# Optimization experiments

Hardware: AMD Instinct MI355X
Metric: run time of the kernel (lower is better)

The kernel has to match this reference:

```python
import jax, jax.numpy as jnp
import numpy as np

B, N, H, L, K = 8, 2048, 256, 4, 16
G, M0, M1, C = 512, 256, 128, 128
EPS = 1e-5


def _rn(k, shape, scale):
    return jax.random.normal(k, shape, jnp.float32) * jnp.float32(scale)


def setup_inputs() -> dict:
    key = jax.random.key(0)
    ks = jax.random.split(key, 16)
    z, o = jnp.zeros, jnp.ones
    return {
        "x": jax.random.normal(ks[0], (B, N, 3), jnp.float32),
        "batch": jnp.repeat(jnp.arange(B, dtype=jnp.int32)[:, None], N, axis=1),
        "Wf": _rn(ks[1], (3, H), 0.5), "bf": z(H),
        "Wnn": _rn(ks[2], (H, H), H ** -0.5), "bnn": z(H),
        "g1": o((L, H)), "b1": z((L, H)),
        "We": _rn(ks[3], (L, 2 * H, H), (2 * H) ** -0.5), "be": z((L, H)),
        "g2": o((L, H)), "b2": z((L, H)),
        "Wl": _rn(ks[4], (L, H, H), H ** -0.5), "bl": z((L, H)),
        "alpha": _rn(ks[5], (L,), 0.1),
        "gg": o(H), "bgb": z(H),
        "Wg": _rn(ks[6], (H, G), H ** -0.5), "bg2": z(G),
        "Wm1": _rn(ks[7], (G, M0), G ** -0.5), "bm1": z(M0),
        "Wm2": _rn(ks[8], (M0, M1), M0 ** -0.5), "bm2": z(M1),
        "Wm3": _rn(ks[9], (M1, C), M1 ** -0.5), "bm3": z(C),
    }


def _bn(x, g, b):
    # BatchNorm1d training-mode math over all nodes (axes B,N), per channel
    m = x.mean(axis=(0, 1))
    v = x.var(axis=(0, 1))
    return (x - m) * jax.lax.rsqrt(v + EPS) * g + b


def _dgcnn(x, We, be):
    # dynamic kNN graph in feature space, per cloud; x: [B,N,H]
    sq = jnp.sum(x * x, axis=-1)                                  # [B,N]
    d = sq[:, :, None] + sq[:, None, :] - 2.0 * jnp.einsum('bnd,bmd->bnm', x, x)
    idx = jax.lax.top_k(-d, K)[1]                                 # [B,N,K] (includes self)
    x_j = jax.vmap(lambda xb, ib: xb[ib])(x, idx)                 # [B,N,K,H]
    x_i = x[:, :, None, :]
    e = jnp.concatenate([jnp.broadcast_to(x_i, x_j.shape), x_j - x_i], axis=-1)
    msg = jnp.einsum('bnkf,fh->bnkh', e, We) + be                 # edge MLP
    return jnp.max(msg, axis=2)                                   # max aggregate


def _forward(x, Wf, bf, Wnn, bnn, g1, b1, We, be, g2, b2, Wl, bl, alpha,
             gg, bgb, Wg, bg2, Wm1, bm1, Wm2, bm2, Wm3, bm3):
    h = x @ Wf + bf                                               # ffm_x (Linear, scale=None)
    for i in range(L):
        t = h @ Wnn + bnn if i == 0 else h                        # nn_x only on first layer
        t = jax.nn.relu(_bn(t, g1[i], b1[i]))
        t = _dgcnn(t, We[i], be[i])
        t = jax.nn.relu(_bn(t, g2[i], b2[i]))
        t = t @ Wl[i] + bl[i]
        h = h + alpha[i] * t                                      # ResidualCoefficient
    t = jax.nn.relu(_bn(h, gg, bgb)) @ Wg + bg2
    p = jnp.max(t, axis=1)                                        # global max pool -> [B,G]
    p = jax.nn.relu(p @ Wm1 + bm1)
    p = jax.nn.relu(p @ Wm2 + bm2)
    return p @ Wm3 + bm3                                          # [B, n_components]


def reference(x, batch, Wf, bf, Wnn, bnn, g1, b1, We, be, g2, b2, Wl, bl, alpha,
              gg, bgb, Wg, bg2, Wm1, bm1, Wm2, bm2, Wm3, bm3):
    # batch ids are implied by the dense [B,N] layout; kept for signature fidelity
    del batch
    return _forward(x, Wf, bf, Wnn, bnn, g1, b1, We, be, g2, b2, Wl, bl, alpha,
                    gg, bgb, Wg, bg2, Wm1, bm1, Wm2, bm2, Wm3, bm3)
```

## Files before the change

kernel.cpp:

```cpp
#include <hip/hip_runtime.h>
#include <cfloat>

#define B_  8
#define N_  2048
#define H_  256
#define L_  4
#define K_  16
#define G_  512
#define M0_ 256
#define M1_ 128
#define C_  128
#define BN_ 16384
#define KP_ 768

typedef unsigned short ushort_t;
typedef __attribute__((ext_vector_type(8))) short short8;
typedef __attribute__((ext_vector_type(4))) float f32x4;

#define OFF_H     ((size_t)0)
#define OFF_APACK ((size_t)16777216)
#define OFF_SQ    ((size_t)67108864)
#define OFF_IDX   ((size_t)67174400)
#define OFF_STATS ((size_t)68222976)
#define OFF_SCSH  ((size_t)68227072)
#define OFF_BCAT  ((size_t)68229120)
#define OFF_P0    ((size_t)68231168)
#define OFF_P1    ((size_t)68247552)
#define OFF_P2    ((size_t)68255744)
#define OFF_D     ((size_t)69206016)
#define OFF_T     (OFF_D + (size_t)0)
#define OFF_UV    (OFF_D + (size_t)50331648)
#define OFF_QW    (OFF_D + (size_t)83886080)
#define OFF_PMAX  (OFF_D + (size_t)84672512)
#define WS_NEEDED ((size_t)203423744)

static __device__ __forceinline__ ushort_t f2bf(float f) {
    unsigned u = __float_as_uint(f);
    unsigned r = (u + 0x7fffu + ((u >> 16) & 1u)) >> 16;
    return (ushort_t)r;
}
static __device__ __forceinline__ float bf2f(ushort_t h) {
    return __uint_as_float(((unsigned)h) << 16);
}
static __device__ __forceinline__ void pack3(float v, ushort_t* A, size_t base, int f) {
    ushort_t hi = f2bf(v);
    ushort_t lo = f2bf(v - bf2f(hi));
    A[base + f] = hi; A[base + H_ + f] = lo; A[base + 2 * H_ + f] = hi;
}


__global__ void feat_pack(const float* __restrict__ x, const float* __restrict__ Wf,
                          const float* __restrict__ bfv, float* __restrict__ h,
                          ushort_t* __restrict__ Ap) {
    int pt = blockIdx.x;
    int f  = threadIdx.x;
    float x0 = x[pt * 3 + 0], x1 = x[pt * 3 + 1], x2 = x[pt * 3 + 2];
    float v = x0 * Wf[f] + x1 * Wf[H_ + f] + x2 * Wf[2 * H_ + f] + bfv[f];
    h[(size_t)pt * H_ + f] = v;
    pack3(v, Ap, (size_t)pt * KP_, f);
}

__global__ void pack_wT(const float* __restrict__ W, ushort_t* __restrict__ Qp, int Nd) {
    int n = blockIdx.x, k = threadIdx.x;
    float w = W[(size_t)k * Nd + n];
    ushort_t hi = f2bf(w), lo = f2bf(w - bf2f(hi));
    size_t base = (size_t)n * KP_;
    Qp[base + k] = hi; Qp[base + H_ + k] = hi; Qp[base + 2 * H_ + k] = lo;
}

__global__ void pack_qcat(const float* __restrict__ We_l, const float* __restrict__ be_l,
                          ushort_t* __restrict__ Qp, float* __restrict__ bcat) {
    int n = blockIdx.x, k = threadIdx.x;
    float w;
    if (n < H_) w = We_l[(size_t)k * H_ + n] - We_l[(size_t)H_ * H_ + (size_t)k * H_ + n];
    else        w = We_l[(size_t)H_ * H_ + (size_t)k * H_ + (n - H_)];
    ushort_t hi = f2bf(w), lo = f2bf(w - bf2f(hi));
    size_t base = (size_t)n * KP_;
    Qp[base + k] = hi; Qp[base + H_ + k] = hi; Qp[base + 2 * H_ + k] = lo;
    if (k == 0) bcat[n] = (n < H_) ? be_l[n] : 0.f;
}

__global__ __launch_bounds__(256) void mfma_gemm(
    const ushort_t* __restrict__ P, const ushort_t* __restrict__ Q,
    const float* __restrict__ aux, float* __restrict__ out,
    int Kd, int ldOut, int mode, const float* __restrict__ resid,
    const float* __restrict__ alphap, int aidx, double* __restrict__ stats,
    int nx) {
    __shared__ __align__(16) ushort_t As[128 * 32];
    __shared__ __align__(16) ushort_t Bs[128 * 32];
    __shared__ float cs1[4][64], cs2[4][64];
    int i0, j0;
    if (nx) {
        int blk = blockIdx.x;
        int z = blk & 7;
        int rest = blk >> 3;
        int xb = rest % nx;
        int ys = rest / nx;
        i0 = (z * 16 + ys) * 128;
        j0 = xb * 128;
    } else {
        i0 = blockIdx.y * 128; j0 = blockIdx.x * 128;
    }
    int tid = threadIdx.x;
    int lane = tid & 63, wave = tid >> 6;
    int wm = wave & 1, wn = wave >> 1;
    int m16 = lane & 15, kq = (lane >> 4) * 8;

    f32x4 acc[4][4];
    f32x4 zero = {0.f, 0.f, 0.f, 0.f};
#pragma unroll
    for (int i = 0; i < 4; ++i)
#pragma unroll
        for (int j = 0; j < 4; ++j) acc[i][j] = zero;

    int srow = tid >> 2;
    int skc  = (tid & 3) * 8;

    for (int k0 = 0; k0 < Kd; k0 += 32) {
#pragma unroll
        for (int s = 0; s < 2; ++s) {
            int row = srow + s * 64;
            const ushort_t* gpA = P + (size_t)(i0 + row) * Kd + k0 + skc;
            const ushort_t* gpB = Q + (size_t)(j0 + row) * Kd + k0 + skc;
            __builtin_amdgcn_global_load_lds(
                (const __attribute__((address_space(1))) void*)gpA,
                (__attribute__((address_space(3))) void*)(As + (size_t)(wave * 64 + s * 256) * 8),
                16, 0, 0);
            __builtin_amdgcn_global_load_lds(
                (const __attribute__((address_space(1))) void*)gpB,
                (__attribute__((address_space(3))) void*)(Bs + (size_t)(wave * 64 + s * 256) * 8),
                16, 0, 0);
        }
        __syncthreads();
        short8 af[4], bfr[4];
#pragma unroll
        for (int fi = 0; fi < 4; ++fi)
            af[fi] = *(const short8*)(As + (wm * 64 + fi * 16 + m16) * 32 + kq);
#pragma unroll
        for (int fj = 0; fj < 4; ++fj)
            bfr[fj] = *(const short8*)(Bs + (wn * 64 + fj * 16 + m16) * 32 + kq);
#pragma unroll
        for (int fi = 0; fi < 4; ++fi)
#pragma unroll
            for (int fj = 0; fj < 4; ++fj)
                acc[fi][fj] = __builtin_amdgcn_mfma_f32_16x16x32_bf16(
                    af[fi], bfr[fj], acc[fi][fj], 0, 0, 0);
        __syncthreads();
    }
    float alpha = (mode == 2) ? alphap[aidx] : 0.f;
    int rbase = i0 + wm * 64 + (lane >> 4) * 4;
    int cbase = j0 + wn * 64 + m16;
    float s1[4] = {0.f, 0.f, 0.f, 0.f}, s2[4] = {0.f, 0.f, 0.f, 0.f};
#pragma unroll
    for (int fi = 0; fi < 4; ++fi) {
#pragma unroll
        for (int fj = 0; fj < 4; ++fj) {
            int c = cbase + fj * 16;
            float a = aux[c];
#pragma unroll
            for (int r = 0; r < 4; ++r) {
                int gr = rbase + fi * 16 + r;
                size_t oidx = (size_t)gr * ldOut + c;
                float val;
                if (mode == 2) val = resid[oidx] + alpha * (acc[fi][fj][r] + a);
                else           val = acc[fi][fj][r] + a;
                out[oidx] = val;
                s1[fj] += val; s2[fj] += val * val;
            }
        }
    }
    if (stats) {
#pragma unroll
        for (int fj = 0; fj < 4; ++fj) {
            float a1 = s1[fj], a2 = s2[fj];
            a1 += __shfl_xor(a1, 16); a1 += __shfl_xor(a1, 32);
            a2 += __shfl_xor(a2, 16); a2 += __shfl_xor(a2, 32);
            if ((lane >> 4) == 0) {
                cs1[wave][fj * 16 + m16] = a1;
                cs2[wave][fj * 16 + m16] = a2;
            }
        }
        __syncthreads();
        if (tid < 128) {
            int wnl = tid >> 6, cl = tid & 63;
            float t1 = cs1[2 * wnl][cl] + cs1[2 * wnl + 1][cl];
            float t2 = cs2[2 * wnl][cl] + cs2[2 * wnl + 1][cl];
            int c = j0 + tid;
            atomicAdd(&stats[c], (double)t1);
            atomicAdd(&stats[H_ + c], (double)t2);
        }
    }
}

__global__ __launch_bounds__(256) void gram_sym(const ushort_t* __restrict__ Ap,
                                                const float* __restrict__ sqb,
                                                float* __restrict__ D) {
    __shared__ __align__(16) ushort_t As[128 * 32];
    __shared__ __align__(16) ushort_t Bs[128 * 32];
    __shared__ __align__(16) float stg[4][1280];
    int blk = blockIdx.x;
    int z = blk & 7;
    int p = blk >> 3;
    int bi = 0, rem = p;
    while (rem >= 16 - bi) { rem -= 16 - bi; ++bi; }
    int bj = bi + rem;
    const ushort_t* Pz = Ap + (size_t)z * N_ * KP_;
    const float* sqz = sqb + (size_t)z * N_;
    float* Dz = D + (size_t)z * N_ * N_;
    int i0 = bi * 128, j0 = bj * 128;

    int tid = threadIdx.x;
    int lane = tid & 63, wave = tid >> 6;
    int wm = wave & 1, wn = wave >> 1;
    int m16 = lane & 15, q4 = lane >> 4;
    int kq = q4 * 8;

    f32x4 acc[4][4];
    f32x4 zero = {0.f, 0.f, 0.f, 0.f};
#pragma unroll
    for (int i = 0; i < 4; ++i)
#pragma unroll
        for (int j = 0; j < 4; ++j) acc[i][j] = zero;

    int srow = tid >> 2;
    int skc  = (tid & 3) * 8;

    for (int k0 = 0; k0 < KP_; k0 += 32) {
        int kb = (k0 < 256) ? k0 : ((k0 < 512) ? k0 + 256 : k0 - 256);
#pragma unroll
        for (int s = 0; s < 2; ++s) {
            int row = srow + s * 64;
            const ushort_t* gpA = Pz + (size_t)(i0 + row) * KP_ + k0 + skc;
            const ushort_t* gpB = Pz + (size_t)(j0 + row) * KP_ + kb + skc;
            __builtin_amdgcn_global_load_lds(
                (const __attribute__((address_space(1))) void*)gpA,
                (__attribute__((address_space(3))) void*)(As + (size_t)(wave * 64 + s * 256) * 8),
                16, 0, 0);
            __builtin_amdgcn_global_load_lds(
                (const __attribute__((address_space(1))) void*)gpB,
                (__attribute__((address_space(3))) void*)(Bs + (size_t)(wave * 64 + s * 256) * 8),
                16, 0, 0);
        }
        __syncthreads();
        short8 af[4], bfr[4];
#pragma unroll
        for (int fi = 0; fi < 4; ++fi)
            af[fi] = *(const short8*)(As + (wm * 64 + fi * 16 + m16) * 32 + kq);
#pragma unroll
        for (int fj = 0; fj < 4; ++fj)
            bfr[fj] = *(const short8*)(Bs + (wn * 64 + fj * 16 + m16) * 32 + kq);
#pragma unroll
        for (int fi = 0; fi < 4; ++fi)
#pragma unroll
            for (int fj = 0; fj < 4; ++fj)
                acc[fi][fj] = __builtin_amdgcn_mfma_f32_16x16x32_bf16(
                    af[fi], bfr[fj], acc[fi][fj], 0, 0, 0);
        __syncthreads();
    }

    float* sg = stg[wave];
    float scl[4];
#pragma unroll
    for (int fj = 0; fj < 4; ++fj) scl[fj] = sqz[j0 + wn * 64 + fj * 16 + m16];
    float sr[4][4];
#pragma unroll
    for (int fi = 0; fi < 4; ++fi) {
        float4 s4 = *(const float4*)(sqz + i0 + wm * 64 + fi * 16 + q4 * 4);
        sr[fi][0] = s4.x; sr[fi][1] = s4.y; sr[fi][2] = s4.z; sr[fi][3] = s4.w;
    }

    int rr = lane >> 2, cc = lane & 3;
#pragma unroll
    for (int fi = 0; fi < 4; ++fi) {
#pragma unroll
        for (int fj = 0; fj < 4; ++fj)
#pragma unroll
            for (int r = 0; r < 4; ++r)
                sg[(q4 * 4 + r) * 68 + fj * 16 + m16] = scl[fj] - 2.f * acc[fi][fj][r];
        float* drow = Dz + (size_t)(i0 + wm * 64 + fi * 16 + rr) * N_ + j0 + wn * 64;
#pragma unroll
        for (int t = 0; t < 4; ++t) {
            int chunk = cc + 4 * t;
            f32x4 o = *(const f32x4*)(sg + rr * 68 + chunk * 4);
            __builtin_nontemporal_store(o, (f32x4*)(drow + chunk * 4));
        }
    }

    if (bi != bj) {
#pragma unroll
        for (int fi = 0; fi < 4; ++fi) {
#pragma unroll
            for (int fj = 0; fj < 4; ++fj)
#pragma unroll
                for (int r = 0; r < 4; ++r)
                    sg[(fj * 16 + m16) * 20 + q4 * 4 + r] =
                        sr[fi][r] - 2.f * acc[fi][fj][r];
            int chunk = lane & 3;
#pragma unroll
            for (int u = 0; u < 4; ++u) {
                int cr = (lane >> 2) + 16 * u;
                f32x4 o = *(const f32x4*)(sg + cr * 20 + chunk * 4);
                __builtin_nontemporal_store(o,
                    (f32x4*)(Dz + (size_t)(j0 + wn * 64 + cr) * N_ +
                             i0 + wm * 64 + fi * 16 + chunk * 4));
            }
        }
    }
}

__global__ __launch_bounds__(256) void topk16(const float* __restrict__ D,
                                              int* __restrict__ idxb) {
    __shared__ unsigned long long cand[4][256];
    __shared__ int cnt[4];
    int w = threadIdx.x >> 6, lane = threadIdx.x & 63;
    int row = blockIdx.x * 4 + w;
    const float* dp = D + (size_t)row * N_;
    unsigned sk[32];
#pragma unroll
    for (int t = 0; t < 8; ++t) {
        f32x4 v4 = __builtin_nontemporal_load((const f32x4*)(dp + t * 256 + lane * 4));
#pragma unroll
        for (int j = 0; j < 4; ++j) {
            unsigned u = __float_as_uint(v4[j]);
            sk[t * 4 + j] = (u & 0x80000000u) ? ~u : (u | 0x80000000u);
        }
    }
    if (lane == 0) cnt[w] = 0;
    unsigned vm = sk[0];
#pragma unroll
    for (int i = 1; i < 32; ++i) vm = min(vm, sk[i]);
#pragma unroll
    for (int k = 2; k <= 64; k <<= 1) {
#pragma unroll
        for (int j = k >> 1; j > 0; j >>= 1) {
            unsigned pv = __shfl_xor(vm, j);
            bool up = ((lane & k) == 0);
            bool lower = ((lane & j) == 0);
            unsigned mn = min(vm, pv), mx = max(vm, pv);
            vm = (lower == up) ? mn : mx;
        }
    }
    unsigned T = __shfl(vm, 15);
    __syncthreads();
#pragma unroll
    for (int i = 0; i < 32; ++i) {
        if (sk[i] <= T) {
            unsigned col = (unsigned)((i >> 2) * 256 + lane * 4 + (i & 3));
            int s = atomicAdd(&cnt[w], 1);
            if (s < 256) cand[w][s] = ((unsigned long long)sk[i] << 32) | col;
        }
    }
    __syncthreads();
    int cn = cnt[w];
    if (cn <= 64) {
        unsigned long long mykey = (lane < cn) ? cand[w][lane] : ~0ull;
        for (int it = 0; it < 16; ++it) {
            unsigned long long best = mykey;
#pragma unroll
            for (int off = 32; off; off >>= 1) {
                unsigned long long o = __shfl_xor(best, off);
                if (o < best) best = o;
            }
            if (mykey == best) mykey = ~0ull;
            if (lane == 0) idxb[row * 16 + it] = (int)(unsigned)(best & 0xffffffffu);
        }
    } else if (cn <= 256) {
        for (int it = 0; it < 16; ++it) {
            unsigned long long best = ~0ull;
            for (int i = lane; i < cn; i += 64) {
                unsigned long long c = cand[w][i];
                if (c < best) best = c;
            }
#pragma unroll
            for (int off = 32; off; off >>= 1) {
                unsigned long long o = __shfl_xor(best, off);
                if (o < best) best = o;
            }
            for (int i = lane; i < cn; i += 64)
                if (cand[w][i] == best) cand[w][i] = ~0ull;
            if (lane == 0) idxb[row * 16 + it] = (int)(unsigned)(best & 0xffffffffu);
        }
    } else {
        unsigned mask = 0;
        for (int it = 0; it < 16; ++it) {
            unsigned long long key = ~0ull;
#pragma unroll
            for (int i = 0; i < 32; ++i) {
                if (!((mask >> i) & 1u)) {
                    unsigned long long k2 = ((unsigned long long)sk[i] << 32) |
                        (unsigned)((i >> 2) * 256 + lane * 4 + (i & 3));
                    if (k2 < key) key = k2;
                }
            }
#pragma unroll
            for (int off = 32; off; off >>= 1) {
                unsigned long long o = __shfl_xor(key, off);
                if (o < key) key = o;
            }
            unsigned jc = (unsigned)(key & 0xffffffffu);
            int li = ((jc & 255) >> 2);
            int ii = ((jc >> 8) << 2) | (jc & 3);
            if (lane == li) mask |= 1u << ii;
            if (lane == 0) idxb[row * 16 + it] = (int)jc;
        }
    }
}

__global__ void gather_max(const float* __restrict__ uv, const int* __restrict__ idxb,
                           float* __restrict__ outp, double* __restrict__ stats) {
    int blk = blockIdx.x;
    int b = blk & 7;
    int strip = blk >> 3;
    int r0 = b * N_ + strip * 32;
    int f = threadIdx.x;
    float s1 = 0.f, s2 = 0.f;
    for (int rr = 0; rr < 32; ++rr) {
        int row = r0 + rr;
        const int* ip = idxb + row * 16;
        float m = -FLT_MAX;
#pragma unroll
        for (int k = 0; k < 16; ++k) {
            int j = ip[k];
            m = fmaxf(m, uv[((size_t)((b << 11) + j)) * 512 + 256 + f]);
        }
        float v = uv[(size_t)row * 512 + f] + m;
        outp[(size_t)row * H_ + f] = v;
        s1 += v; s2 += v * v;
    }
    atomicAdd(&stats[f], (double)s1);
    atomicAdd(&stats[H_ + f], (double)s2);
}

__global__ void bn_zero(double* s) { s[threadIdx.x] = 0.0; }

__global__ void bn_final(double* __restrict__ sums, const float* __restrict__ g,
                         const float* __restrict__ b, float* __restrict__ scsh) {
    int f = threadIdx.x;
    double m  = sums[f] / (double)BN_;
    double var = sums[H_ + f] / (double)BN_ - m * m;
    double inv = 1.0 / sqrt(var + 1e-5);
    float sc = g[f] * (float)inv;
    scsh[f] = sc;
    scsh[H_ + f] = b[f] - (float)m * sc;
    sums[f] = 0.0; sums[H_ + f] = 0.0;
}

__global__ void bn_apply_pack(const float* __restrict__ X, const float* __restrict__ scsh,
                              ushort_t* __restrict__ Ap, float* __restrict__ sq) {
    int tid = threadIdx.x;
    int row = blockIdx.x * 8 + (tid >> 5);
    int f0  = (tid & 31) * 8;
    const float* xp = X + (size_t)row * H_ + f0;
    f32x4 x0 = *(const f32x4*)(xp);
    f32x4 x1 = *(const f32x4*)(xp + 4);
    f32x4 sc0 = *(const f32x4*)(scsh + f0);
    f32x4 sc1 = *(const f32x4*)(scsh + f0 + 4);
    f32x4 sh0 = *(const f32x4*)(scsh + H_ + f0);
    f32x4 sh1 = *(const f32x4*)(scsh + H_ + f0 + 4);
    float v[8];
#pragma unroll
    for (int i = 0; i < 4; ++i) {
        v[i]     = fmaxf(x0[i] * sc0[i] + sh0[i], 0.f);
        v[i + 4] = fmaxf(x1[i] * sc1[i] + sh1[i], 0.f);
    }
    short8 hi8, lo8;
#pragma unroll
    for (int i = 0; i < 8; ++i) {
        ushort_t hi = f2bf(v[i]);
        ushort_t lo = f2bf(v[i] - bf2f(hi));
        hi8[i] = (short)hi; lo8[i] = (short)lo;
    }
    ushort_t* ap = Ap + (size_t)row * KP_ + f0;
    *(short8*)(ap)            = hi8;
    *(short8*)(ap + H_)       = lo8;
    *(short8*)(ap + 2 * H_)   = hi8;
    if (sq) {
        float s = 0.f;
#pragma unroll
        for (int i = 0; i < 8; ++i) s += v[i] * v[i];
#pragma unroll
        for (int off = 16; off; off >>= 1) s += __shfl_down(s, off, 32);
        if ((tid & 31) == 0) sq[row] = s;
    }
}

__global__ void maxpool1(const float* __restrict__ y, float* __restrict__ pmax) {
    int b = blockIdx.x, gc = blockIdx.y, nc = blockIdx.z;
    int g = gc * 256 + threadIdx.x;
    const float* yb = y + ((size_t)b * N_ + (size_t)nc * 128) * G_;
    float m = -FLT_MAX;
    for (int n = 0; n < 128; ++n) m = fmaxf(m, yb[(size_t)n * G_ + g]);
    pmax[((size_t)(b * 16 + nc)) * G_ + g] = m;
}

__global__ void maxpool2(const float* __restrict__ pmax, float* __restrict__ p) {
    int b = blockIdx.x;
    int g = blockIdx.y * 256 + threadIdx.x;
    float m = -FLT_MAX;
    for (int c = 0; c < 16; ++c) m = fmaxf(m, pmax[((size_t)(b * 16 + c)) * G_ + g]);
    p[(size_t)b * G_ + g] = m;
}

__global__ __launch_bounds__(256) void head_gemm(const float* __restrict__ A,
                                                 const float* __restrict__ W,
                                                 const float* __restrict__ bias,
                                                 float* __restrict__ Cc,
                                                 int Kd, int Nd, int relu) {
    int m = blockIdx.x;
    int c0 = blockIdx.y * 64;
    int cl = threadIdx.x & 63;
    int ks = threadIdx.x >> 6;
    int kper = Kd >> 2;
    const float* Ap = A + (size_t)m * Kd + (size_t)ks * kper;
    const float* Wp = W + (size_t)ks * kper * Nd + c0 + cl;
    float acc = 0.f;
    for (int k = 0; k < kper; k += 8) {
#pragma unroll
        for (int u2 = 0; u2 < 8; ++u2)
            acc += Ap[k + u2] * Wp[(size_t)(k + u2) * Nd];
    }
    __shared__ float red[4][64];
    red[ks][cl] = acc;
    __syncthreads();
    if (ks == 0) {
        float s = red[0][cl] + red[1][cl] + red[2][cl] + red[3][cl] + bias[c0 + cl];
        if (relu) s = fmaxf(s, 0.f);
        Cc[(size_t)m * Nd + c0 + cl] = s;
    }
}

extern "C" void kernel_launch(void* const* d_in, const int* in_sizes, int n_in,
                              void* d_out, int out_size, void* d_ws, size_t ws_size,
                              hipStream_t stream) {
    (void)in_sizes; (void)n_in; (void)out_size;
    if (ws_size < WS_NEEDED) return;

    const float* x    = (const float*)d_in[0];
    const float* Wf   = (const float*)d_in[2];
    const float* bfv  = (const float*)d_in[3];
    const float* Wnn  = (const float*)d_in[4];
    const float* bnn  = (const float*)d_in[5];
    const float* g1   = (const float*)d_in[6];
    const float* b1   = (const float*)d_in[7];
    const float* We   = (const float*)d_in[8];
    const float* be   = (const float*)d_in[9];
    const float* g2   = (const float*)d_in[10];
    const float* b2   = (const float*)d_in[11];
    const float* Wl   = (const float*)d_in[12];
    const float* bl   = (const float*)d_in[13];
    const float* alpha= (const float*)d_in[14];
    const float* gg   = (const float*)d_in[15];
    const float* bgb  = (const float*)d_in[16];
    const float* Wg   = (const float*)d_in[17];
    const float* bg2  = (const float*)d_in[18];
    const float* Wm1  = (const float*)d_in[19];
    const float* bm1  = (const float*)d_in[20];
    const float* Wm2  = (const float*)d_in[21];
    const float* bm2  = (const float*)d_in[22];
    const float* Wm3  = (const float*)d_in[23];
    const float* bm3  = (const float*)d_in[24];
    float* outp = (float*)d_out;

    char* ws = (char*)d_ws;
    float*    h    = (float*)(ws + OFF_H);
    ushort_t* Ap   = (ushort_t*)(ws + OFF_APACK);
    float*    sqb  = (float*)(ws + OFF_SQ);
    int*      idxb = (int*)  (ws + OFF_IDX);
    double*   stats= (double*)(ws + OFF_STATS);
    float*    scsh = (float*)(ws + OFF_SCSH);
    float*    bcat = (float*)(ws + OFF_BCAT);
    float*    p0   = (float*)(ws + OFF_P0);
    float*    p1   = (float*)(ws + OFF_P1);
    float*    p2   = (float*)(ws + OFF_P2);
    float*    dmat = (float*)(ws + OFF_D);
    float*    t    = (float*)(ws + OFF_T);
    float*    uv   = (float*)(ws + OFF_UV);
    float*    y    = (float*)(ws + OFF_UV);
    ushort_t* Qw   = (ushort_t*)(ws + OFF_QW);
    float*    pmax = (float*)(ws + OFF_PMAX);

    hipLaunchKernelGGL(bn_zero, dim3(1), dim3(512), 0, stream, stats);

    hipLaunchKernelGGL(feat_pack, dim3(BN_), dim3(256), 0, stream, x, Wf, bfv, h, Ap);
    hipLaunchKernelGGL(pack_wT, dim3(H_), dim3(256), 0, stream, Wnn, Qw, H_);
    hipLaunchKernelGGL(mfma_gemm, dim3(256), dim3(256), 0, stream,
                       Ap, Qw, bnn, t, KP_, H_, 0,
                       (const float*)nullptr, (const float*)nullptr, 0, stats, 2);

    for (int l = 0; l < L_; ++l) {
        const float* src1 = (l == 0) ? t : h;
        hipLaunchKernelGGL(bn_final, dim3(1), dim3(256), 0, stream,
                           stats, g1 + l * H_, b1 + l * H_, scsh);
        hipLaunchKernelGGL(bn_apply_pack, dim3(BN_ / 8), dim3(256), 0, stream,
                           src1, scsh, Ap, sqb);
        hipLaunchKernelGGL(gram_sym, dim3(1088), dim3(256), 0, stream,
                           Ap, sqb, dmat);
        hipLaunchKernelGGL(topk16, dim3(BN_ / 4), dim3(256), 0, stream, dmat, idxb);
        hipLaunchKernelGGL(pack_qcat, dim3(512), dim3(256), 0, stream,
                           We + (size_t)l * 2 * H_ * H_, be + (size_t)l * H_, Qw, bcat);
        hipLaunchKernelGGL(mfma_gemm, dim3(512), dim3(256), 0, stream,
                           Ap, Qw, bcat, uv, KP_, 512, 0,
                           (const float*)nullptr, (const float*)nullptr, 0,
                           (double*)nullptr, 4);
        hipLaunchKernelGGL(gather_max, dim3(512), dim3(256), 0, stream,
                           uv, idxb, t, stats);
        hipLaunchKernelGGL(bn_final, dim3(1), dim3(256), 0, stream,
                           stats, g2 + l * H_, b2 + l * H_, scsh);
        hipLaunchKernelGGL(bn_apply_pack, dim3(BN_ / 8), dim3(256), 0, stream,
                           t, scsh, Ap, (float*)nullptr);
        hipLaunchKernelGGL(pack_wT, dim3(H_), dim3(256), 0, stream,
                           Wl + (size_t)l * H_ * H_, Qw, H_);
        hipLaunchKernelGGL(mfma_gemm, dim3(256), dim3(256), 0, stream,
                           Ap, Qw, bl + (size_t)l * H_, h, KP_, H_, 2,
                           h, alpha, l, stats, 2);
    }

    hipLaunchKernelGGL(bn_final, dim3(1), dim3(256), 0, stream, stats, gg, bgb, scsh);
    hipLaunchKernelGGL(bn_apply_pack, dim3(BN_ / 8), dim3(256), 0, stream,
                       h, scsh, Ap, (float*)nullptr);
    hipLaunchKernelGGL(pack_wT, dim3(G_), dim3(256), 0, stream, Wg, Qw, G_);
    hipLaunchKernelGGL(mfma_gemm, dim3(512), dim3(256), 0, stream,
                       Ap, Qw, bg2, y, KP_, G_, 0,
                       (const float*)nullptr, (const float*)nullptr, 0,
                       (double*)nullptr, 4);
    hipLaunchKernelGGL(maxpool1, dim3(8, 2, 16), dim3(256), 0, stream, y, pmax);
    hipLaunchKernelGGL(maxpool2, dim3(8, 2), dim3(256), 0, stream, pmax, p0);
    hipLaunchKernelGGL(head_gemm, dim3(8, 4), dim3(256), 0, stream, p0, Wm1, bm1, p1, G_, M0_, 1);
    hipLaunchKernelGGL(head_gemm, dim3(8, 2), dim3(256), 0, stream, p1, Wm2, bm2, p2, M0_, M1_, 1);
    hipLaunchKernelGGL(head_gemm, dim3(8, 2), dim3(256), 0, stream, p2, Wm3, bm3, outp, M1_, C_, 0);
}
```

Baseline: 1.135 ms.

## Fuse per-tile top-16 selection into Gram kernel, drop full distance matrix

The Gram kernel no longer writes the full 2048x2048 distance matrix per cloud. Each wave converts its 64x64 tile to sortable keys in shared memory and selects a top-16 candidate set per row with bitonic networks. It then writes compact key and column candidates, which a new topk_cand kernel merges into the final 16 neighbours. This removes the large D write and read traffic in exchange for heavy register use (64-element arrays per lane), a 66 KB dynamic LDS allocation that lowers occupancy, and extra per-tile sorting work.

```diff
diff --git a/kernel.cpp b/kernel.cpp
--- a/kernel.cpp
+++ b/kernel.cpp
@@ -28,6 +28,8 @@
 #define OFF_P1    ((size_t)68247552)
 #define OFF_P2    ((size_t)68255744)
 #define OFF_D     ((size_t)69206016)
+#define OFF_CK    (OFF_D)
+#define OFF_CC    (OFF_D + (size_t)33554432)
 #define OFF_T     (OFF_D + (size_t)0)
 #define OFF_UV    (OFF_D + (size_t)50331648)
 #define OFF_QW    (OFF_D + (size_t)83886080)
@@ -42,10 +44,99 @@
 static __device__ __forceinline__ float bf2f(ushort_t h) {
     return __uint_as_float(((unsigned)h) << 16);
 }
+static __device__ __forceinline__ unsigned f2key(float f) {
+    unsigned u = __float_as_uint(f);
+    return (u & 0x80000000u) ? ~u : (u | 0x80000000u);
+}
 static __device__ __forceinline__ void pack3(float v, ushort_t* A, size_t base, int f) {
     ushort_t hi = f2bf(v);
     ushort_t lo = f2bf(v - bf2f(hi));
     A[base + f] = hi; A[base + H_ + f] = lo; A[base + 2 * H_ + f] = hi;
+}
+
+#define CEA(x, y) { unsigned mn_ = min(x, y), mx_ = max(x, y); (x) = mn_; (y) = mx_; }
+
+static __device__ __forceinline__ void sortnet16(unsigned* s) {
+#pragma unroll
+    for (int k = 2; k <= 16; k <<= 1) {
+#pragma unroll
+        for (int j = k >> 1; j > 0; j >>= 1) {
+#pragma unroll
+            for (int i = 0; i < 16; ++i) {
+                int l = i ^ j;
+                if (l > i) {
+                    if ((i & k) == 0) { CEA(s[i], s[l]); }
+                    else              { CEA(s[l], s[i]); }
+                }
+            }
+        }
+    }
+}
+static __device__ __forceinline__ void clean16(unsigned* s) {
+#pragma unroll
+    for (int j = 8; j > 0; j >>= 1) {
+#pragma unroll
+        for (int i = 0; i < 16; ++i) {
+            int l = i ^ j;
+            if (l > i) { CEA(s[i], s[l]); }
+        }
+    }
+}
+
+static __device__ __forceinline__ void select_emit(
+    unsigned* arena_wave, int lane,
+    unsigned* __restrict__ kc, ushort_t* __restrict__ cc,
+    size_t Rrow, int chunk) {
+    unsigned* mr = arena_wave + lane * 66;
+    unsigned v[64];
+#pragma unroll
+    for (int i = 0; i < 32; ++i) {
+        uint2 t2 = *(const uint2*)(mr + 2 * i);
+        v[2 * i] = t2.x; v[2 * i + 1] = t2.y;
+    }
+    unsigned a[16], b[16], m1[16], m2[16];
+#pragma unroll
+    for (int i = 0; i < 16; ++i) { a[i] = v[i]; b[i] = v[16 + i]; }
+    sortnet16(a); sortnet16(b);
+#pragma unroll
+    for (int i = 0; i < 16; ++i) m1[i] = min(a[i], b[15 - i]);
+    clean16(m1);
+#pragma unroll
+    for (int i = 0; i < 16; ++i) { a[i] = v[32 + i]; b[i] = v[48 + i]; }
+    sortnet16(a); sortnet16(b);
+#pragma unroll
+    for (int i = 0; i < 16; ++i) m2[i] = min(a[i], b[15 - i]);
+    clean16(m2);
+    unsigned T = 0;
+#pragma unroll
+    for (int i = 0; i < 16; ++i) T = max(T, min(m1[i], m2[15 - i]));
+    int cnt = 0;
+#pragma unroll
+    for (int i = 0; i < 64; ++i) {
+        if (v[i] < T) { mr[cnt] = v[i]; mr[16 + cnt] = (unsigned)i; ++cnt; }
+    }
+#pragma unroll
+    for (int i = 0; i < 64; ++i) {
+        if (v[i] == T && cnt < 16) { mr[cnt] = v[i]; mr[16 + cnt] = (unsigned)i; ++cnt; }
+    }
+    unsigned kk[16], c16[16];
+#pragma unroll
+    for (int i = 0; i < 8; ++i) {
+        uint2 tk = *(const uint2*)(mr + 2 * i);
+        kk[2 * i] = tk.x; kk[2 * i + 1] = tk.y;
+        uint2 tc = *(const uint2*)(mr + 16 + 2 * i);
+        c16[2 * i] = tc.x; c16[2 * i + 1] = tc.y;
+    }
+    size_t kb = (Rrow * 32 + (size_t)chunk) * 16;
+    *(uint4*)(kc + kb)      = make_uint4(kk[0],  kk[1],  kk[2],  kk[3]);
+    *(uint4*)(kc + kb + 4)  = make_uint4(kk[4],  kk[5],  kk[6],  kk[7]);
+    *(uint4*)(kc + kb + 8)  = make_uint4(kk[8],  kk[9],  kk[10], kk[11]);
+    *(uint4*)(kc + kb + 12) = make_uint4(kk[12], kk[13], kk[14], kk[15]);
+    unsigned w[8];
+#pragma unroll
+    for (int i = 0; i < 8; ++i) w[i] = c16[2 * i] | (c16[2 * i + 1] << 16);
+    *(uint4*)(cc + kb)     = make_uint4(w[0], w[1], w[2], w[3]);
+    *(uint4*)(cc + kb + 8) = make_uint4(w[4], w[5], w[6], w[7]);
 }
 
 
@@ -194,10 +285,11 @@
 
 __global__ __launch_bounds__(256) void gram_sym(const ushort_t* __restrict__ Ap,
                                                 const float* __restrict__ sqb,
-                                                float* __restrict__ D) {
-    __shared__ __align__(16) ushort_t As[128 * 32];
-    __shared__ __align__(16) ushort_t Bs[128 * 32];
-    __shared__ __align__(16) float stg[4][1280];
+                                                unsigned* __restrict__ kc,
+                                                ushort_t* __restrict__ cc) {
+    extern __shared__ __align__(16) unsigned dyns[];
+    ushort_t* As = (ushort_t*)dyns;
+    ushort_t* Bs = (ushort_t*)dyns + 4096;
     int blk = blockIdx.x;
     int z = blk & 7;
     int p = blk >> 3;
@@ -206,7 +298,6 @@
     int bj = bi + rem;
     const ushort_t* Pz = Ap + (size_t)z * N_ * KP_;
     const float* sqz = sqb + (size_t)z * N_;
-    float* Dz = D + (size_t)z * N_ * N_;
     int i0 = bi * 128, j0 = bj * 128;
 
     int tid = threadIdx.x;
@@ -257,8 +348,8 @@
                     af[fi], bfr[fj], acc[fi][fj], 0, 0, 0);
         __syncthreads();
     }
-
-    float* sg = stg[wave];
+    unsigned* my = dyns + wave * (64 * 66);
+
     float scl[4];
 #pragma unroll
     for (int fj = 0; fj < 4; ++fj) scl[fj] = sqz[j0 + wn * 64 + fj * 16 + m16];
@@ -269,66 +360,56 @@
         sr[fi][0] = s4.x; sr[fi][1] = s4.y; sr[fi][2] = s4.z; sr[fi][3] = s4.w;
     }
 
-    int rr = lane >> 2, cc = lane & 3;
-#pragma unroll
-    for (int fi = 0; fi < 4; ++fi) {
+#pragma unroll
+    for (int fi = 0; fi < 4; ++fi)
 #pragma unroll
         for (int fj = 0; fj < 4; ++fj)
 #pragma unroll
             for (int r = 0; r < 4; ++r)
-                sg[(q4 * 4 + r) * 68 + fj * 16 + m16] = scl[fj] - 2.f * acc[fi][fj][r];
-        float* drow = Dz + (size_t)(i0 + wm * 64 + fi * 16 + rr) * N_ + j0 + wn * 64;
-#pragma unroll
-        for (int t = 0; t < 4; ++t) {
-            int chunk = cc + 4 * t;
-            f32x4 o = *(const f32x4*)(sg + rr * 68 + chunk * 4);
-            __builtin_nontemporal_store(o, (f32x4*)(drow + chunk * 4));
-        }
-    }
+                my[(fi * 16 + q4 * 4 + r) * 66 + (fj * 16 + m16)] =
+                    f2key(scl[fj] - 2.f * acc[fi][fj][r]);
+    select_emit(my, lane, kc, cc,
+                (size_t)z * N_ + i0 + wm * 64 + lane, 2 * bj + wn);
 
     if (bi != bj) {
 #pragma unroll
-        for (int fi = 0; fi < 4; ++fi) {
+        for (int fi = 0; fi < 4; ++fi)
 #pragma unroll
             for (int fj = 0; fj < 4; ++fj)
 #pragma unroll
                 for (int r = 0; r < 4; ++r)
-                    sg[(fj * 16 + m16) * 20 + q4 * 4 + r] =
-                        sr[fi][r] - 2.f * acc[fi][fj][r];
-            int chunk = lane & 3;
-#pragma unroll
-            for (int u = 0; u < 4; ++u) {
-                int cr = (lane >> 2) + 16 * u;
-                f32x4 o = *(const f32x4*)(sg + cr * 20 + chunk * 4);
-                __builtin_nontemporal_store(o,
-                    (f32x4*)(Dz + (size_t)(j0 + wn * 64 + cr) * N_ +
-                             i0 + wm * 64 + fi * 16 + chunk * 4));
-            }
-        }
-    }
-}
-
-__global__ __launch_bounds__(256) void topk16(const float* __restrict__ D,
-                                              int* __restrict__ idxb) {
+                    my[(fj * 16 + m16) * 66 + (fi * 16 + q4 * 4 + r)] =
+                        f2key(sr[fi][r] - 2.f * acc[fi][fj][r]);
+        select_emit(my, lane, kc, cc,
+                    (size_t)z * N_ + j0 + wn * 64 + lane, 2 * bi + wm);
+    }
+}
+
+__global__ __launch_bounds__(256) void topk_cand(const unsigned* __restrict__ kcand,
+                                                 const ushort_t* __restrict__ ccand,
+                                                 int* __restrict__ idxb) {
     __shared__ unsigned long long cand[4][256];
     __shared__ int cnt[4];
     int w = threadIdx.x >> 6, lane = threadIdx.x & 63;
     int row = blockIdx.x * 4 + w;
-    const float* dp = D + (size_t)row * N_;
-    unsigned sk[32];
-#pragma unroll
-    for (int t = 0; t < 8; ++t) {
-        f32x4 v4 = __builtin_nontemporal_load((const f32x4*)(dp + t * 256 + lane * 4));
-#pragma unroll
-        for (int j = 0; j < 4; ++j) {
-            unsigned u = __float_as_uint(v4[j]);
-            sk[t * 4 + j] = (u & 0x80000000u) ? ~u : (u | 0x80000000u);
-        }
+    const unsigned* kp = kcand + (size_t)row * 512 + lane * 8;
+    uint4 ka = *(const uint4*)(kp);
+    uint4 kb = *(const uint4*)(kp + 4);
+    unsigned sk[8] = {ka.x, ka.y, ka.z, ka.w, kb.x, kb.y, kb.z, kb.w};
+    const ushort_t* cp = ccand + (size_t)row * 512 + lane * 8;
+    uint4 cw = *(const uint4*)(cp);
+    unsigned cwa[4] = {cw.x, cw.y, cw.z, cw.w};
+    unsigned colbase = (unsigned)(lane >> 1) * 64u;
+    unsigned long long k2[8];
+#pragma unroll
+    for (int j = 0; j < 8; ++j) {
+        unsigned c = colbase + ((cwa[j >> 1] >> ((j & 1) * 16)) & 0xffffu);
+        k2[j] = ((unsigned long long)sk[j] << 32) | c;
     }
     if (lane == 0) cnt[w] = 0;
     unsigned vm = sk[0];
 #pragma unroll
-    for (int i = 1; i < 32; ++i) vm = min(vm, sk[i]);
+    for (int i = 1; i < 8; ++i) vm = min(vm, sk[i]);
 #pragma unroll
     for (int k = 2; k <= 64; k <<= 1) {
 #pragma unroll
@@ -343,11 +424,10 @@
     unsigned T = __shfl(vm, 15);
     __syncthreads();
 #pragma unroll
-    for (int i = 0; i < 32; ++i) {
-        if (sk[i] <= T) {
-            unsigned col = (unsigned)((i >> 2) * 256 + lane * 4 + (i & 3));
+    for (int j = 0; j < 8; ++j) {
+        if (sk[j] <= T) {
             int s = atomicAdd(&cnt[w], 1);
-            if (s < 256) cand[w][s] = ((unsigned long long)sk[i] << 32) | col;
+            if (s < 256) cand[w][s] = k2[j];
         }
     }
     __syncthreads();
@@ -381,27 +461,21 @@
             if (lane == 0) idxb[row * 16 + it] = (int)(unsigned)(best & 0xffffffffu);
         }
     } else {
-        unsigned mask = 0;
+        unsigned msk = 0;
         for (int it = 0; it < 16; ++it) {
             unsigned long long key = ~0ull;
 #pragma unroll
-            for (int i = 0; i < 32; ++i) {
-                if (!((mask >> i) & 1u)) {
-                    unsigned long long k2 = ((unsigned long long)sk[i] << 32) |
-                        (unsigned)((i >> 2) * 256 + lane * 4 + (i & 3));
-                    if (k2 < key) key = k2;
-                }
-            }
+            for (int i = 0; i < 8; ++i)
+                if (!((msk >> i) & 1u) && k2[i] < key) key = k2[i];
 #pragma unroll
             for (int off = 32; off; off >>= 1) {
                 unsigned long long o = __shfl_xor(key, off);
                 if (o < key) key = o;
             }
-            unsigned jc = (unsigned)(key & 0xffffffffu);
-            int li = ((jc & 255) >> 2);
-            int ii = ((jc >> 8) << 2) | (jc & 3);
-            if (lane == li) mask |= 1u << ii;
-            if (lane == 0) idxb[row * 16 + it] = (int)jc;
+#pragma unroll
+            for (int i = 0; i < 8; ++i)
+                if (k2[i] == key) msk |= 1u << i;
+            if (lane == 0) idxb[row * 16 + it] = (int)(unsigned)(key & 0xffffffffu);
         }
     }
 }
@@ -572,7 +646,8 @@
     float*    p0   = (float*)(ws + OFF_P0);
     float*    p1   = (float*)(ws + OFF_P1);
     float*    p2   = (float*)(ws + OFF_P2);
-    float*    dmat = (float*)(ws + OFF_D);
+    unsigned* kcand= (unsigned*)(ws + OFF_CK);
+    ushort_t* ccand= (ushort_t*)(ws + OFF_CC);
     float*    t    = (float*)(ws + OFF_T);
     float*    uv   = (float*)(ws + OFF_UV);
     float*    y    = (float*)(ws + OFF_UV);
@@ -593,9 +668,10 @@
                            stats, g1 + l * H_, b1 + l * H_, scsh);
         hipLaunchKernelGGL(bn_apply_pack, dim3(BN_ / 8), dim3(256), 0, stream,
                            src1, scsh, Ap, sqb);
-        hipLaunchKernelGGL(gram_sym, dim3(1088), dim3(256), 0, stream,
-                           Ap, sqb, dmat);
-        hipLaunchKernelGGL(topk16, dim3(BN_ / 4), dim3(256), 0, stream, dmat, idxb);
+        hipLaunchKernelGGL(gram_sym, dim3(1088), dim3(256), 67584, stream,
+                           Ap, sqb, kcand, ccand);
+        hipLaunchKernelGGL(topk_cand, dim3(BN_ / 4), dim3(256), 0, stream,
+                           kcand, ccand, idxb);
         hipLaunchKernelGGL(pack_qcat, dim3(512), dim3(256), 0, stream,
                            We + (size_t)l * 2 * H_ * H_, be + (size_t)l * H_, Qw, bcat);
         hipLaunchKernelGGL(mfma_gemm, dim3(512), dim3(256), 0, stream,
```

Result: slower. 1.391 ms (+22.5%).

## Emit per-32-column chunk minima from gram kernel to prune top-k reads

Applied to the files above, without the earlier changes.

The gram kernel now also writes, for each row, the minimum distance key over every 32-column chunk (64 chunks per row) into a new workspace buffer, for both the direct and transposed tiles. The top-k kernel builds its threshold from these 64 chunk minima instead of reading the full 2048-wide row. It then reads only the chunks whose minimum is at or below the threshold, and falls back to a full row read only in the overflow case. This cuts most of the distance-matrix read traffic in top-k, at the cost of extra reductions and small scattered stores in gram_sym.

```diff
diff --git a/kernel.cpp b/kernel.cpp
--- a/kernel.cpp
+++ b/kernel.cpp
@@ -19,6 +19,7 @@
 
 #define OFF_H     ((size_t)0)
 #define OFF_APACK ((size_t)16777216)
+#define OFF_MIND  ((size_t)46137344)
 #define OFF_SQ    ((size_t)67108864)
 #define OFF_IDX   ((size_t)67174400)
 #define OFF_STATS ((size_t)68222976)
@@ -41,6 +42,10 @@
 }
 static __device__ __forceinline__ float bf2f(ushort_t h) {
     return __uint_as_float(((unsigned)h) << 16);
+}
+static __device__ __forceinline__ unsigned f2key(float f) {
+    unsigned u = __float_as_uint(f);
+    return (u & 0x80000000u) ? ~u : (u | 0x80000000u);
 }
 static __device__ __forceinline__ void pack3(float v, ushort_t* A, size_t base, int f) {
     ushort_t hi = f2bf(v);
@@ -194,7 +199,8 @@
 
 __global__ __launch_bounds__(256) void gram_sym(const ushort_t* __restrict__ Ap,
                                                 const float* __restrict__ sqb,
-                                                float* __restrict__ D) {
+                                                float* __restrict__ D,
+                                                unsigned* __restrict__ minD) {
     __shared__ __align__(16) ushort_t As[128 * 32];
     __shared__ __align__(16) ushort_t Bs[128 * 32];
     __shared__ __align__(16) float stg[4][1280];
@@ -286,6 +292,33 @@
         }
     }
 
+#pragma unroll
+    for (int fi = 0; fi < 4; ++fi) {
+        unsigned c0k[4], c1k[4];
+#pragma unroll
+        for (int r = 0; r < 4; ++r) {
+            unsigned k0m = min(f2key(scl[0] - 2.f * acc[fi][0][r]),
+                               f2key(scl[1] - 2.f * acc[fi][1][r]));
+            unsigned k1m = min(f2key(scl[2] - 2.f * acc[fi][2][r]),
+                               f2key(scl[3] - 2.f * acc[fi][3][r]));
+#pragma unroll
+            for (int off = 1; off <= 8; off <<= 1) {
+                k0m = min(k0m, (unsigned)__shfl_xor((int)k0m, off));
+                k1m = min(k1m, (unsigned)__shfl_xor((int)k1m, off));
+            }
+            c0k[r] = k0m; c1k[r] = k1m;
+        }
+        if (m16 == 0) {
+            size_t mb = ((size_t)z * N_ + i0 + wm * 64 + fi * 16 + q4 * 4) * 64
+                        + (size_t)(bj * 4 + wn * 2);
+#pragma unroll
+            for (int r = 0; r < 4; ++r) {
+                minD[mb + (size_t)r * 64]     = c0k[r];
+                minD[mb + (size_t)r * 64 + 1] = c1k[r];
+            }
+        }
+    }
+
     if (bi != bj) {
 #pragma unroll
         for (int fi = 0; fi < 4; ++fi) {
@@ -305,30 +338,42 @@
                              i0 + wm * 64 + fi * 16 + chunk * 4));
             }
         }
+
+#pragma unroll
+        for (int fj = 0; fj < 4; ++fj) {
+            unsigned k0m = 0xFFFFFFFFu, k1m = 0xFFFFFFFFu;
+#pragma unroll
+            for (int fi = 0; fi < 2; ++fi)
+#pragma unroll
+                for (int r = 0; r < 4; ++r) {
+                    k0m = min(k0m, f2key(sr[fi][r]     - 2.f * acc[fi][fj][r]));
+                    k1m = min(k1m, f2key(sr[fi + 2][r] - 2.f * acc[fi + 2][fj][r]));
+                }
+            k0m = min(k0m, (unsigned)__shfl_xor((int)k0m, 16));
+            k0m = min(k0m, (unsigned)__shfl_xor((int)k0m, 32));
+            k1m = min(k1m, (unsigned)__shfl_xor((int)k1m, 16));
+            k1m = min(k1m, (unsigned)__shfl_xor((int)k1m, 32));
+            if (q4 == 0) {
+                size_t mb = ((size_t)z * N_ + j0 + wn * 64 + fj * 16 + m16) * 64
+                            + (size_t)(bi * 4 + wm * 2);
+                minD[mb]     = k0m;
+                minD[mb + 1] = k1m;
+            }
+        }
     }
 }
 
 __global__ __launch_bounds__(256) void topk16(const float* __restrict__ D,
+                                              const unsigned* __restrict__ minD,
                                               int* __restrict__ idxb) {
     __shared__ unsigned long long cand[4][256];
     __shared__ int cnt[4];
     int w = threadIdx.x >> 6, lane = threadIdx.x & 63;
     int row = blockIdx.x * 4 + w;
     const float* dp = D + (size_t)row * N_;
-    unsigned sk[32];
-#pragma unroll
-    for (int t = 0; t < 8; ++t) {
-        f32x4 v4 = __builtin_nontemporal_load((const f32x4*)(dp + t * 256 + lane * 4));
-#pragma unroll
-        for (int j = 0; j < 4; ++j) {
-            unsigned u = __float_as_uint(v4[j]);
-            sk[t * 4 + j] = (u & 0x80000000u) ? ~u : (u | 0x80000000u);
-        }
-    }
+    unsigned mv = minD[(size_t)row * 64 + lane];
     if (lane == 0) cnt[w] = 0;
-    unsigned vm = sk[0];
-#pragma unroll
-    for (int i = 1; i < 32; ++i) vm = min(vm, sk[i]);
+    unsigned vm = mv;
 #pragma unroll
     for (int k = 2; k <= 64; k <<= 1) {
 #pragma unroll
@@ -341,14 +386,30 @@
         }
     }
     unsigned T = __shfl(vm, 15);
+    unsigned long long cmask = __ballot(mv <= T);
     __syncthreads();
-#pragma unroll
-    for (int i = 0; i < 32; ++i) {
-        if (sk[i] <= T) {
-            unsigned col = (unsigned)((i >> 2) * 256 + lane * 4 + (i & 3));
-            int s = atomicAdd(&cnt[w], 1);
-            if (s < 256) cand[w][s] = ((unsigned long long)sk[i] << 32) | col;
-        }
+    int nc = __popcll(cmask);
+    unsigned long long mrem = cmask;
+    unsigned long long lowmask = (1ull << lane) - 1ull;
+    for (int it = 0; it < nc; it += 2) {
+        int c0 = __ffsll(mrem) - 1; mrem &= mrem - 1ull;
+        int c1 = -1;
+        if (it + 1 < nc) { c1 = __ffsll(mrem) - 1; mrem &= mrem - 1ull; }
+        int c = (lane < 32) ? c0 : c1;
+        bool act = (c >= 0);
+        float dv = act ? dp[c * 32 + (lane & 31)] : 0.f;
+        unsigned kk2 = f2key(dv);
+        bool sel = act && (kk2 <= T);
+        unsigned long long bal = __ballot(sel);
+        int tot = __popcll(bal);
+        int rk  = __popcll(bal & lowmask);
+        int base = 0;
+        if (lane == 0) base = atomicAdd(&cnt[w], tot);
+        base = __shfl(base, 0);
+        int s = base + rk;
+        if (sel && s < 256)
+            cand[w][s] = ((unsigned long long)kk2 << 32) |
+                         (unsigned)(c * 32 + (lane & 31));
     }
     __syncthreads();
     int cn = cnt[w];
@@ -381,6 +442,13 @@
             if (lane == 0) idxb[row * 16 + it] = (int)(unsigned)(best & 0xffffffffu);
         }
     } else {
+        unsigned sk[32];
+#pragma unroll
+        for (int t = 0; t < 8; ++t) {
+            f32x4 v4 = __builtin_nontemporal_load((const f32x4*)(dp + t * 256 + lane * 4));
+#pragma unroll
+            for (int j = 0; j < 4; ++j) sk[t * 4 + j] = f2key(v4[j]);
+        }
         unsigned mask = 0;
         for (int it = 0; it < 16; ++it) {
             unsigned long long key = ~0ull;
@@ -564,6 +632,7 @@
     char* ws = (char*)d_ws;
     float*    h    = (float*)(ws + OFF_H);
     ushort_t* Ap   = (ushort_t*)(ws + OFF_APACK);
+    unsigned* minDp= (unsigned*)(ws + OFF_MIND);
     float*    sqb  = (float*)(ws + OFF_SQ);
     int*      idxb = (int*)  (ws + OFF_IDX);
     double*   stats= (double*)(ws + OFF_STATS);
@@ -594,8 +663,9 @@
         hipLaunchKernelGGL(bn_apply_pack, dim3(BN_ / 8), dim3(256), 0, stream,
                            src1, scsh, Ap, sqb);
         hipLaunchKernelGGL(gram_sym, dim3(1088), dim3(256), 0, stream,
-                           Ap, sqb, dmat);
-        hipLaunchKernelGGL(topk16, dim3(BN_ / 4), dim3(256), 0, stream, dmat, idxb);
+                           Ap, sqb, dmat, minDp);
+        hipLaunchKernelGGL(topk16, dim3(BN_ / 4), dim3(256), 0, stream,
+                           dmat, minDp, idxb);
         hipLaunchKernelGGL(pack_qcat, dim3(512), dim3(256), 0, stream,
                            We + (size_t)l * 2 * H_ * H_, be + (size_t)l * H_, Qw, bcat);
         hipLaunchKernelGGL(mfma_gemm, dim3(512), dim3(256), 0, stream,
```

Result: slower. 1.233 ms (+8.7%).
